# Optimization experiments

Measured on AMD Instinct MI355X. Metric: run time of the kernel, lower is better.

Reference implementation:

```python
import jax, jax.numpy as jnp
import numpy as np

P = 200_000   # pedestrians
T = 16        # frames in targets/outputs
F_DIR = 15    # tracklet_length - 5 frames used by direction loss


def _conv_bbox(b):
    # Faithful to the source's in-place convert_bbox, which (due to sequential
    # in-place updates) maps [a,b,c,d] -> [a-c/2, b-d/2, a, b].
    a, bb, c, d = b[..., 0], b[..., 1], b[..., 2], b[..., 3]
    return jnp.stack([a - 0.5 * c, bb - 0.5 * d, a, bb], axis=-1)


def _corner_pts(b):
    # 5 reference points: center, lt(x0,y0), rt(x0,y1), lb(x1,y0), rb(x1,y1)
    x0, y0, x1, y1 = b[..., 0], b[..., 1], b[..., 2], b[..., 3]
    xs = jnp.stack([0.5 * (x0 + x1), x0, x0, x1, x1], axis=-1)
    ys = jnp.stack([0.5 * (y0 + y1), y0, y1, y0, y1], axis=-1)
    return xs, ys


def _unit_dir(fx, fy, tx, ty):
    dy, dx = ty - fy, tx - fx
    n = jnp.sqrt(dy * dy + dx * dx) + 1e-6
    return dy / n, dx / n


def _direction_loss(outputs, targets):
    last = targets[:F_DIR, :, :4]
    pred = last + outputs[:F_DIR]
    true = targets[1:F_DIR + 1, :, :4]
    # Source mutates `targets` in place: frames 1..14 get convert_bbox applied
    # TWICE when reused as `last_abs` (once as prior frame's true_abs). Replicate.
    last_c1 = _conv_bbox(last)
    last_eff = jnp.concatenate([last_c1[:1], _conv_bbox(last_c1[1:])], axis=0)
    pred_c = _conv_bbox(pred)
    true_c = _conv_bbox(true)
    lx, ly = _corner_pts(last_eff)   # [F_DIR, P, 5]
    px, py = _corner_pts(pred_c)
    tx, ty = _corner_pts(true_c)
    pdy, pdx = _unit_dir(lx, ly, px, py)
    tdy, tdx = _unit_dir(lx, ly, tx, ty)
    cosang = jnp.clip(pdy * tdy + pdx * tdx, -1.0, 1.0)
    weight = 0.2
    return weight * jnp.sum(jnp.arccos(cosang)) / (targets.shape[1] * F_DIR)


def setup_inputs() -> dict:
    key = jax.random.key(0)
    k1, k2 = jax.random.split(key)
    outputs = jax.random.normal(k1, (T, P, 4), dtype=jnp.float32) * 0.1
    targets = jax.random.uniform(k2, (T, P, 8), dtype=jnp.float32)
    return {"outputs": outputs, "targets": targets}


def reference(outputs, targets):
    delta = targets[:, :, 4:8]
    d = outputs - delta
    ad = jnp.abs(d)
    sl1 = jnp.where(ad < 1.0, 0.5 * d * d, ad - 0.5)  # smooth_l1, beta=1
    loss_o = jnp.sum(sl1, axis=2) / targets.shape[1]   # [T, P]
    loss_dir = _direction_loss(outputs, targets)
    return 0.99 * loss_o + 0.01 * loss_dir
```

## Files before the change

kernel.cpp:

```cpp
#include <hip/hip_runtime.h>

#define BS 256

__device__ __forceinline__ float fast_acos(float x) {
    float ax = fabsf(x);
    float s  = sqrtf(fmaxf(0.f, 1.f - ax));
    float p  = fmaf(ax, fmaf(ax, fmaf(ax, -0.0187293f, 0.0742610f), -0.2121144f), 1.5707288f);
    float r  = s * p;
    return (x >= 0.f) ? r : 3.14159265358979f - r;
}

__device__ __forceinline__ float dir_item(float4 L, float4 O, float4 Tn, bool first) {
    float pa = L.x + O.x, pb = L.y + O.y, pc = L.z + O.z, pd = L.w + O.w;
    float Px0 = pa - 0.5f * pc, Py0 = pb - 0.5f * pd, Px1 = pa, Py1 = pb;
    float Tx0 = Tn.x - 0.5f * Tn.z, Ty0 = Tn.y - 0.5f * Tn.w, Tx1 = Tn.x, Ty1 = Tn.y;
    float Lx1 = L.x - 0.5f * L.z, Ly1 = L.y - 0.5f * L.w;
    float Lx0, Ly0;
    if (first) { Lx0 = Lx1; Ly0 = Ly1; Lx1 = L.x; Ly1 = L.y; }
    else       { Lx0 = 0.5f * (L.x - L.z); Ly0 = 0.5f * (L.y - L.w); }

    float lxs[5] = {0.5f * (Lx0 + Lx1), Lx0, Lx0, Lx1, Lx1};
    float lys[5] = {0.5f * (Ly0 + Ly1), Ly0, Ly1, Ly0, Ly1};
    float pxs[5] = {0.5f * (Px0 + Px1), Px0, Px0, Px1, Px1};
    float pys[5] = {0.5f * (Py0 + Py1), Py0, Py1, Py0, Py1};
    float txs[5] = {0.5f * (Tx0 + Tx1), Tx0, Tx0, Tx1, Tx1};
    float tys[5] = {0.5f * (Ty0 + Ty1), Ty0, Ty1, Ty0, Ty1};

    float acc = 0.f;
    #pragma unroll
    for (int k = 0; k < 5; ++k) {
        float pdx = pxs[k] - lxs[k], pdy = pys[k] - lys[k];
        float tdx = txs[k] - lxs[k], tdy = tys[k] - lys[k];
        float p2  = pdx * pdx + pdy * pdy;
        float t2  = tdx * tdx + tdy * tdy;
        float dot = pdx * tdx + pdy * tdy;
        float inv = rsqrtf(p2 * t2);
        float cosang = fminf(1.0f, fmaxf(-1.0f, dot * inv));
        acc += fast_acos(cosang);
    }
    return acc;
}

__device__ __forceinline__ float sl1_4(float4 O, float4 D) {
    float s = 0.f;
    { float d = O.x - D.x, ad = fabsf(d); s += (ad < 1.f) ? 0.5f * d * d : ad - 0.5f; }
    { float d = O.y - D.y, ad = fabsf(d); s += (ad < 1.f) ? 0.5f * d * d : ad - 0.5f; }
    { float d = O.z - D.z, ad = fabsf(d); s += (ad < 1.f) ? 0.5f * d * d : ad - 0.5f; }
    { float d = O.w - D.w, ad = fabsf(d); s += (ad < 1.f) ? 0.5f * d * d : ad - 0.5f; }
    return s;
}

#define LD4(ptr) (*reinterpret_cast<const float4*>(ptr))

__global__ __launch_bounds__(BS, 4) __attribute__((amdgpu_waves_per_eu(4, 4)))
void fused_kernel(const float* __restrict__ outputs,
                  const float* __restrict__ targets,
                  float* __restrict__ out,
                  float* __restrict__ partials,
                  int P, float w) {
    __shared__ float smem[BS / 64];
    long long gid = (long long)blockIdx.x * BS + threadIdx.x;
    float acc = 0.f;
    if (gid < 4ll * P) {
        int grp     = (int)(gid / P);
        long long p = gid - (long long)grp * P;
        const long long ts8 = 8ll * P, os4 = 4ll * P;
        const float* tb = targets + ((long long)(grp * 4) * P + p) * 8;
        const float* ob = outputs + ((long long)(grp * 4) * P + p) * 4;
        float*       wb = out + (long long)(grp * 4) * P + p;
        const bool has4 = (grp < 3);

        float4 Tf0 = LD4(tb);
        float4 Tf1 = LD4(tb + ts8);
        float4 Tf2 = LD4(tb + 2 * ts8);
        float4 Tf3 = LD4(tb + 3 * ts8);
        float4 Ts0 = LD4(tb + 4);
        float4 Ts1 = LD4(tb + ts8 + 4);
        float4 Ts2 = LD4(tb + 2 * ts8 + 4);
        float4 Ts3 = LD4(tb + 3 * ts8 + 4);
        float4 O0  = LD4(ob);
        float4 O1  = LD4(ob + os4);
        float4 O2  = LD4(ob + 2 * os4);
        float4 O3  = LD4(ob + 3 * os4);
        float4 Tf4 = has4 ? LD4(tb + 4 * ts8) : make_float4(0.f, 0.f, 0.f, 0.f);

        asm volatile("" ::
            "v"(Tf0.x), "v"(Tf1.x), "v"(Tf2.x), "v"(Tf3.x), "v"(Tf4.x),
            "v"(Ts0.x), "v"(Ts1.x), "v"(Ts2.x), "v"(Ts3.x),
            "v"(O0.x),  "v"(O1.x),  "v"(O2.x),  "v"(O3.x));

        wb[0]       = sl1_4(O0, Ts0) * w;
        wb[P]       = sl1_4(O1, Ts1) * w;
        wb[2ll * P] = sl1_4(O2, Ts2) * w;
        wb[3ll * P] = sl1_4(O3, Ts3) * w;

        acc  = dir_item(Tf0, O0, Tf1, grp == 0);
        acc += dir_item(Tf1, O1, Tf2, false);
        acc += dir_item(Tf2, O2, Tf3, false);
        if (has4) acc += dir_item(Tf3, O3, Tf4, false);
    }
    #pragma unroll
    for (int off = 32; off > 0; off >>= 1) acc += __shfl_down(acc, off, 64);
    int lane = threadIdx.x & 63, w64 = threadIdx.x >> 6;
    if (lane == 0) smem[w64] = acc;
    __syncthreads();
    if (threadIdx.x == 0) {
        float r = 0.f;
        #pragma unroll
        for (int i = 0; i < BS / 64; ++i) r += smem[i];
        partials[blockIdx.x] = r;
    }
}

__global__ void finalize_kernel(const float* __restrict__ partials, int nb,
                                float* __restrict__ out, long long n4, int P) {
    __shared__ double dsm[BS / 64];
    __shared__ float c_sh;
    double dacc = 0.0;
    for (int i = threadIdx.x; i < nb; i += BS) dacc += (double)partials[i];
    #pragma unroll
    for (int off = 32; off > 0; off >>= 1) dacc += __shfl_down(dacc, off, 64);
    int lane = threadIdx.x & 63, w = threadIdx.x >> 6;
    if (lane == 0) dsm[w] = dacc;
    __syncthreads();
    if (threadIdx.x == 0) {
        double tot = dsm[0] + dsm[1] + dsm[2] + dsm[3];
        c_sh = (float)(0.01 * 0.2 * tot / ((double)P * 15.0));
    }
    __syncthreads();
    float c = c_sh;

    float4* o4 = reinterpret_cast<float4*>(out);
    long long stride = (long long)gridDim.x * blockDim.x;
    for (long long i = (long long)blockIdx.x * blockDim.x + threadIdx.x; i < n4; i += stride) {
        float4 v = o4[i];
        v.x += c; v.y += c; v.z += c; v.w += c;
        o4[i] = v;
    }
}

extern "C" void kernel_launch(void* const* d_in, const int* in_sizes, int n_in,
                              void* d_out, int out_size, void* d_ws, size_t ws_size,
                              hipStream_t stream) {
    const float* outputs = (const float*)d_in[0];
    const float* targets = (const float*)d_in[1];
    float* out = (float*)d_out;
    float* partials = (float*)d_ws;

    const int T = 16;
    int P = in_sizes[0] / (T * 4);

    long long nthreads = 4ll * P;
    int nb1 = (int)((nthreads + BS - 1) / BS);
    fused_kernel<<<nb1, BS, 0, stream>>>(outputs, targets, out, partials,
                                         P, 0.99f / (float)P);

    long long n4 = (long long)out_size / 4;
    int nb2 = (int)((n4 + BS - 1) / BS);
    if (nb2 > 2048) nb2 = 2048;
    finalize_kernel<<<nb2, BS, 0, stream>>>(partials, nb1, out, n4, P);
}
```

Baseline: 45.14 us.

## Stage tile inputs through LDS via async global_load_lds with swizzled layout

Replaces per-thread direct float4 global loads with a cooperative tile staging scheme: each block loads a 256-pedestrian tile of targets and outputs into LDS using global_load_lds 16-byte transfers, with an XOR swizzle to avoid bank conflicts, then each thread reads its values from LDS. Blocks are remapped to (group, pedestrian tile) pairs and the occupancy hint is relaxed to allow the large LDS allocation. The intent is more coalesced, fully contiguous global reads and fewer VGPRs tied up in outstanding loads. In exchange it adds about 56KB of LDS per block, which limits occupancy, plus a full wait-and-barrier before any compute starts, so load and compute no longer overlap within a block.

Measured after the change: 46.52 us. 3.0% more time.

```diff
diff --git a/kernel.cpp b/kernel.cpp
--- a/kernel.cpp
+++ b/kernel.cpp
@@ -1,6 +1,15 @@
 #include <hip/hip_runtime.h>
 
 #define BS 256
+#define TILE 256
+
+__device__ __forceinline__ int sw(int c) { return c ^ ((c >> 3) & 7); }
+
+__device__ __forceinline__ void gload_lds16(const float* g, float* l) {
+    __builtin_amdgcn_global_load_lds(
+        (const __attribute__((address_space(1))) void*)g,
+        (__attribute__((address_space(3))) void*)l, 16, 0, 0);
+}
 
 __device__ __forceinline__ float fast_acos(float x) {
     float ax = fabsf(x);
@@ -50,66 +59,89 @@
     return s;
 }
 
-#define LD4(ptr) (*reinterpret_cast<const float4*>(ptr))
-
-__global__ __launch_bounds__(BS, 4) __attribute__((amdgpu_waves_per_eu(4, 4)))
+__global__ __launch_bounds__(BS, 2)
 void fused_kernel(const float* __restrict__ outputs,
                   const float* __restrict__ targets,
                   float* __restrict__ out,
                   float* __restrict__ partials,
-                  int P, float w) {
+                  int P, int npb, float w) {
+    __shared__ float lds[14336];
     __shared__ float smem[BS / 64];
-    long long gid = (long long)blockIdx.x * BS + threadIdx.x;
+
+    int g  = blockIdx.x / npb;
+    int pb = blockIdx.x - g * npb;
+    int p0 = pb * TILE;
+    int Pv = P - p0; if (Pv > TILE) Pv = TILE;
+    const long long ts8 = 8ll * P, os4 = 4ll * P;
+    const float* gT = targets + ((long long)(4 * g) * P + p0) * 8;
+    const float* gO = outputs + ((long long)(4 * g) * P + p0) * 4;
+    const int wv = threadIdx.x >> 6, lane = threadIdx.x & 63;
+    const bool has4 = (g < 3);
+
+    const int tcmax = 2 * Pv - 1;
+    #pragma unroll
+    for (int r = 0; r < 4; ++r) {
+        #pragma unroll
+        for (int k = 0; k < 2; ++k) {
+            int q = wv * 128 + k * 64 + lane;
+            int c = sw(q); if (c > tcmax) c = tcmax;
+            gload_lds16(gT + r * ts8 + c * 4, &lds[(r * 512 + q) * 4]);
+        }
+    }
+    if (has4) {
+        #pragma unroll
+        for (int k = 0; k < 2; ++k) {
+            int q = wv * 128 + k * 64 + lane;
+            int c = sw(q); if (c > tcmax) c = tcmax;
+            gload_lds16(gT + 4 * ts8 + c * 4, &lds[(4 * 512 + q) * 4]);
+        }
+    }
+    const int ocmax = Pv - 1;
+    #pragma unroll
+    for (int r = 0; r < 4; ++r) {
+        int q = wv * 64 + lane;
+        int c = sw(q); if (c > ocmax) c = ocmax;
+        gload_lds16(gO + r * os4 + c * 4, &lds[(2560 + r * 256 + q) * 4]);
+    }
+    asm volatile("s_waitcnt vmcnt(0)" ::: "memory");
+    __syncthreads();
+
     float acc = 0.f;
-    if (gid < 4ll * P) {
-        int grp     = (int)(gid / P);
-        long long p = gid - (long long)grp * P;
-        const long long ts8 = 8ll * P, os4 = 4ll * P;
-        const float* tb = targets + ((long long)(grp * 4) * P + p) * 8;
-        const float* ob = outputs + ((long long)(grp * 4) * P + p) * 4;
-        float*       wb = out + (long long)(grp * 4) * P + p;
-        const bool has4 = (grp < 3);
+    int i = threadIdx.x;
+    if (i < Pv) {
+        float4 Tf0 = *(float4*)&lds[(0 * 512 + sw(2 * i)) * 4];
+        float4 Ts0 = *(float4*)&lds[(0 * 512 + sw(2 * i + 1)) * 4];
+        float4 Tf1 = *(float4*)&lds[(1 * 512 + sw(2 * i)) * 4];
+        float4 Ts1 = *(float4*)&lds[(1 * 512 + sw(2 * i + 1)) * 4];
+        float4 Tf2 = *(float4*)&lds[(2 * 512 + sw(2 * i)) * 4];
+        float4 Ts2 = *(float4*)&lds[(2 * 512 + sw(2 * i + 1)) * 4];
+        float4 Tf3 = *(float4*)&lds[(3 * 512 + sw(2 * i)) * 4];
+        float4 Ts3 = *(float4*)&lds[(3 * 512 + sw(2 * i + 1)) * 4];
+        float4 O0  = *(float4*)&lds[(2560 + 0 * 256 + sw(i)) * 4];
+        float4 O1  = *(float4*)&lds[(2560 + 1 * 256 + sw(i)) * 4];
+        float4 O2  = *(float4*)&lds[(2560 + 2 * 256 + sw(i)) * 4];
+        float4 O3  = *(float4*)&lds[(2560 + 3 * 256 + sw(i)) * 4];
+        float4 Tf4 = has4 ? *(float4*)&lds[(4 * 512 + sw(2 * i)) * 4]
+                          : make_float4(0.f, 0.f, 0.f, 0.f);
 
-        float4 Tf0 = LD4(tb);
-        float4 Tf1 = LD4(tb + ts8);
-        float4 Tf2 = LD4(tb + 2 * ts8);
-        float4 Tf3 = LD4(tb + 3 * ts8);
-        float4 Ts0 = LD4(tb + 4);
-        float4 Ts1 = LD4(tb + ts8 + 4);
-        float4 Ts2 = LD4(tb + 2 * ts8 + 4);
-        float4 Ts3 = LD4(tb + 3 * ts8 + 4);
-        float4 O0  = LD4(ob);
-        float4 O1  = LD4(ob + os4);
-        float4 O2  = LD4(ob + 2 * os4);
-        float4 O3  = LD4(ob + 3 * os4);
-        float4 Tf4 = has4 ? LD4(tb + 4 * ts8) : make_float4(0.f, 0.f, 0.f, 0.f);
-
-        asm volatile("" ::
-            "v"(Tf0.x), "v"(Tf1.x), "v"(Tf2.x), "v"(Tf3.x), "v"(Tf4.x),
-            "v"(Ts0.x), "v"(Ts1.x), "v"(Ts2.x), "v"(Ts3.x),
-            "v"(O0.x),  "v"(O1.x),  "v"(O2.x),  "v"(O3.x));
-
+        float* wb = out + (long long)(4 * g) * P + p0 + i;
         wb[0]       = sl1_4(O0, Ts0) * w;
         wb[P]       = sl1_4(O1, Ts1) * w;
         wb[2ll * P] = sl1_4(O2, Ts2) * w;
         wb[3ll * P] = sl1_4(O3, Ts3) * w;
 
-        acc  = dir_item(Tf0, O0, Tf1, grp == 0);
+        acc  = dir_item(Tf0, O0, Tf1, g == 0);
         acc += dir_item(Tf1, O1, Tf2, false);
         acc += dir_item(Tf2, O2, Tf3, false);
         if (has4) acc += dir_item(Tf3, O3, Tf4, false);
     }
+
     #pragma unroll
     for (int off = 32; off > 0; off >>= 1) acc += __shfl_down(acc, off, 64);
-    int lane = threadIdx.x & 63, w64 = threadIdx.x >> 6;
-    if (lane == 0) smem[w64] = acc;
+    if (lane == 0) smem[wv] = acc;
     __syncthreads();
-    if (threadIdx.x == 0) {
-        float r = 0.f;
-        #pragma unroll
-        for (int i = 0; i < BS / 64; ++i) r += smem[i];
-        partials[blockIdx.x] = r;
-    }
+    if (threadIdx.x == 0)
+        partials[blockIdx.x] = smem[0] + smem[1] + smem[2] + smem[3];
 }
 
 __global__ void finalize_kernel(const float* __restrict__ partials, int nb,
@@ -149,11 +181,11 @@
 
     const int T = 16;
     int P = in_sizes[0] / (T * 4);
+    int npb = (P + TILE - 1) / TILE;
+    int nb1 = 4 * npb;
 
-    long long nthreads = 4ll * P;
-    int nb1 = (int)((nthreads + BS - 1) / BS);
     fused_kernel<<<nb1, BS, 0, stream>>>(outputs, targets, out, partials,
-                                         P, 0.99f / (float)P);
+                                         P, npb, 0.99f / (float)P);
 
     long long n4 = (long long)out_size / 4;
     int nb2 = (int)((n4 + BS - 1) / BS);
```
